# Kernel tuning notes

Hardware: AMD Instinct MI355X
Metric: run time of the kernel (lower is better)

The kernel has to match this reference:

```python
import jax, jax.numpy as jnp
import numpy as np

B, T, D, H = 4, 2048, 1024, 16
HD = D // H  # 64


def setup_inputs() -> dict:
    key = jax.random.key(0)
    k1, k2, k3 = jax.random.split(key, 3)
    x = jax.random.normal(k1, (B, T, D), dtype=jnp.float32)
    # xavier-uniform-ish scaling for stability
    W_qkv = jax.random.normal(k2, (3 * D, D), dtype=jnp.float32) * (1.0 / np.sqrt(D))
    W_proj = jax.random.normal(k3, (D, D), dtype=jnp.float32) * (1.0 / np.sqrt(D))
    b_proj = jnp.zeros((D,), dtype=jnp.float32)
    return {"x": x, "W_qkv": W_qkv, "W_proj": W_proj, "b_proj": b_proj}


def reference(x, W_qkv, W_proj, b_proj):
    Bx, Tx, C = x.shape
    qkv = x @ W_qkv.T                      # [B,T,3C]
    q, k, v = jnp.split(qkv, 3, axis=-1)
    # [B,T,C] -> [B,H,T,hd]
    def heads(t):
        return t.reshape(Bx, Tx, H, HD).transpose(0, 2, 1, 3)
    q, k, v = heads(q), heads(k), heads(v)
    scale = 1.0 / np.sqrt(HD)
    scores = jnp.einsum('bhqd,bhkd->bhqk', q, k) * scale  # [B,H,T,T]
    causal = jnp.tril(jnp.ones((Tx, Tx), dtype=bool))
    scores = jnp.where(causal, scores, jnp.finfo(scores.dtype).min)
    attn = jax.nn.softmax(scores, axis=-1)
    out = jnp.einsum('bhqk,bhkd->bhqd', attn, v)          # [B,H,T,hd]
    out = out.transpose(0, 2, 1, 3).reshape(Bx, Tx, C)    # [B,T,C]
    return out @ W_proj.T + b_proj
```

## Files before the change

kernel.cpp:

```cpp
#include <hip/hip_runtime.h>
#include <hip/hip_bf16.h>

#define B_  4
#define T_  2048
#define D_  1024
#define H_  16
#define HD_ 64
#define THREE_D (3 * D_)
#define TWO_D   (2 * D_)

typedef short s16x8 __attribute__((ext_vector_type(8)));
typedef float f32x4 __attribute__((ext_vector_type(4)));
typedef unsigned short u16;
typedef unsigned short u16x4 __attribute__((ext_vector_type(4)));

static __device__ __forceinline__ s16x8 load8(const u16* p) {
    return *reinterpret_cast<const s16x8*>(p);
}
static __device__ __forceinline__ u16 f2bf(float f) {
    __hip_bfloat16 h = __float2bfloat16(f);
    return *reinterpret_cast<u16*>(&h);
}
static __device__ __forceinline__ u16 bftrunc(float f) {
    unsigned u; __builtin_memcpy(&u, &f, 4); return (u16)(u >> 16);
}

static __device__ __forceinline__ void gload_lds16(const u16* g, u16* l) {
#if __has_builtin(__builtin_amdgcn_global_load_lds)
    __builtin_amdgcn_global_load_lds(
        (__attribute__((address_space(1))) void*)g,
        (__attribute__((address_space(3))) void*)l, 16, 0, 0);
#else
    *reinterpret_cast<s16x8*>(l) = load8(g);
#endif
}

__global__ __launch_bounds__(256) void cvt3_f32_bf16(
    const float* __restrict__ a, u16* __restrict__ oa, int na,
    const float* __restrict__ bsrc, u16* __restrict__ ob, int nb,
    const float* __restrict__ c, u16* __restrict__ oc, int nc)
{
    int i = (blockIdx.x * 256 + threadIdx.x) * 4;
    const float* s; u16* d;
    if (i < na)                { s = a;    d = oa; }
    else if ((i -= na) < nb)   { s = bsrc; d = ob; }
    else if ((i -= nb) < nc)   { s = c;    d = oc; }
    else return;
    const float4 f = *reinterpret_cast<const float4*>(s + i);
    u16x4 r;
    r.x = f2bf(f.x); r.y = f2bf(f.y); r.z = f2bf(f.z); r.w = f2bf(f.w);
    *reinterpret_cast<u16x4*>(d + i) = r;
}

template<int MODE>
__global__ __launch_bounds__(256) void gemm_bt128(
    const u16* __restrict__ A,
    const u16* __restrict__ Bm,
    void* __restrict__ Cv,
    const float* __restrict__ bias,
    int M, int N, int K, int lda, int ldb, int ldc,
    float qsc, u16* __restrict__ vt)
{
    const int ntiles = N >> 7;
    const int mt = blockIdx.x / ntiles;
    const int nt = blockIdx.x % ntiles;
    const int m0 = mt * 128, n0 = nt * 128;
    const int tid  = threadIdx.x;
    const int lane = tid & 63;
    const int l15  = lane & 15;
    const int quad = lane >> 4;
    const int wave = tid >> 6;
    const int wm = (wave >> 1) * 64;
    const int wn = (wave & 1) * 64;

    __shared__ u16 A_sh[2][128 * 32];
    __shared__ u16 B_sh[2][128 * 32];

    f32x4 acc[4][4] = {};

    const int c0 = tid, c1 = tid + 256;
    const int ar0 = c0 >> 2, as0 = (c0 & 3) * 8;
    const int ar1 = c1 >> 2, as1 = (c1 & 3) * 8;
    const u16* Ag0 = A  + (size_t)(m0 + ar0) * lda + as0;
    const u16* Ag1 = A  + (size_t)(m0 + ar1) * lda + as1;
    const u16* Bg0 = Bm + (size_t)(n0 + ar0) * ldb + as0;
    const u16* Bg1 = Bm + (size_t)(n0 + ar1) * ldb + as1;

    for (int k0 = 0; k0 < K; k0 += 64) {
        __syncthreads();
        #pragma unroll
        for (int p = 0; p < 2; ++p) {
            gload_lds16(Ag0 + k0 + p * 32, &A_sh[p][c0 * 8]);
            gload_lds16(Ag1 + k0 + p * 32, &A_sh[p][c1 * 8]);
            gload_lds16(Bg0 + k0 + p * 32, &B_sh[p][c0 * 8]);
            gload_lds16(Bg1 + k0 + p * 32, &B_sh[p][c1 * 8]);
        }
        __syncthreads();

        #pragma unroll
        for (int p = 0; p < 2; ++p) {
            s16x8 a[4], b[4];
            #pragma unroll
            for (int i = 0; i < 4; ++i) {
                a[i] = *reinterpret_cast<const s16x8*>(&A_sh[p][(wm + i * 16 + l15) * 32 + quad * 8]);
                b[i] = *reinterpret_cast<const s16x8*>(&B_sh[p][(wn + i * 16 + l15) * 32 + quad * 8]);
            }
            #pragma unroll
            for (int mi = 0; mi < 4; ++mi)
                #pragma unroll
                for (int ni = 0; ni < 4; ++ni)
                    acc[mi][ni] = __builtin_amdgcn_mfma_f32_16x16x32_bf16(
                        a[mi], b[ni], acc[mi][ni], 0, 0, 0);
        }
    }

    #pragma unroll
    for (int ni = 0; ni < 4; ++ni) {
        const int col = n0 + wn + ni * 16 + l15;
        if (MODE == 0) {
            const float bv = bias ? bias[col] : 0.0f;
            #pragma unroll
            for (int mi = 0; mi < 4; ++mi) {
                const int row = m0 + wm + mi * 16 + quad * 4;
                #pragma unroll
                for (int r = 0; r < 4; ++r)
                    ((float*)Cv)[(size_t)(row + r) * ldc + col] = acc[mi][ni][r] + bv;
            }
        } else {
            if (col < TWO_D) {
                const float sc = (col < D_) ? qsc : 1.0f;
                #pragma unroll
                for (int mi = 0; mi < 4; ++mi) {
                    const int row = m0 + wm + mi * 16 + quad * 4;
                    #pragma unroll
                    for (int r = 0; r < 4; ++r)
                        ((u16*)Cv)[(size_t)(row + r) * ldc + col] = f2bf(acc[mi][ni][r] * sc);
                }
            } else {
                const int vc = col - TWO_D;
                #pragma unroll
                for (int mi = 0; mi < 4; ++mi) {
                    const int row = m0 + wm + mi * 16 + quad * 4;
                    const int bb = row >> 11, t = row & (T_ - 1);
                    u16x4 pk;
                    #pragma unroll
                    for (int r = 0; r < 4; ++r) pk[r] = f2bf(acc[mi][ni][r]);
                    *reinterpret_cast<u16x4*>(
                        vt + ((size_t)(bb * H_ * HD_) + vc) * T_ + t) = pk;
                }
            }
        }
    }
}

__global__ __launch_bounds__(512) void flash_attn11(
    const u16* __restrict__ qk, const u16* __restrict__ vt,
    u16* __restrict__ out)
{
    const int cls = blockIdx.x >> 6;
    const int bh  = blockIdx.x & 63;
    const int qt  = 7 - cls;
    const int h = bh & 15, b = bh >> 4;
    const int q0 = qt * 256;

    __shared__ u16 K_lds[64 * 72];
    __shared__ u16 V_lds[64 * 72];
    __shared__ u16 P_lds[8 * 32 * 72];

    const int tid = threadIdx.x;
    const int wave = tid >> 6, lane = tid & 63;
    const int l15 = lane & 15, quad = lane >> 4;
    u16* Pw = P_lds + wave * (32 * 72);

    const int w0 = q0 + wave * 32;

    s16x8 qf[2][2];
    #pragma unroll
    for (int mi = 0; mi < 2; ++mi) {
        const size_t rowQ = (size_t)(b * T_ + w0 + mi * 16 + l15) * TWO_D + h * HD_;
        qf[mi][0] = load8(qk + rowQ + quad * 8);
        qf[mi][1] = load8(qk + rowQ + 32 + quad * 8);
    }

    f32x4 o[2][4] = {};
    f32x4 osum[2] = {};

    s16x8 ones;
    #pragma unroll
    for (int j = 0; j < 8; ++j) ones[j] = (short)0x3F80;

    const int rk = tid >> 3;
    const int s0 = (tid & 7) * 8;
    const u16* Kg = qk + (size_t)(b * T_ + rk) * TWO_D + D_ + h * HD_ + s0;
    const u16* Vg = vt + (size_t)(bh * HD_ + rk) * T_ + s0;

    s16x8 pk0 = load8(Kg);
    s16x8 pv0 = load8(Vg);

    const int nkt = 4 * qt + 4;
    for (int kt = 0; kt < nkt; ++kt) {
        const int kbase = kt * 64;
        __syncthreads();
        *reinterpret_cast<s16x8*>(&K_lds[rk * 72 + s0]) = pk0;
        *reinterpret_cast<s16x8*>(&V_lds[rk * 72 + s0]) = pv0;
        __syncthreads();

        if (kt + 1 < nkt) {
            const int nb = kbase + 64;
            pk0 = load8(Kg + (size_t)nb * TWO_D);
            pv0 = load8(Vg + nb);
        }

        if (kbase <= w0 + 31) {
            f32x4 st[2][4];
            #pragma unroll
            for (int n = 0; n < 4; ++n) {
                const s16x8 kf0 = *reinterpret_cast<const s16x8*>(
                    &K_lds[(n * 16 + l15) * 72 + quad * 8]);
                const s16x8 kf1 = *reinterpret_cast<const s16x8*>(
                    &K_lds[(n * 16 + l15) * 72 + 32 + quad * 8]);
                #pragma unroll
                for (int mi = 0; mi < 2; ++mi) {
                    f32x4 t = {};
                    t = __builtin_amdgcn_mfma_f32_16x16x32_bf16(kf0, qf[mi][0], t, 0, 0, 0);
                    t = __builtin_amdgcn_mfma_f32_16x16x32_bf16(kf1, qf[mi][1], t, 0, 0, 0);
                    st[mi][n] = t;
                }
            }

            const bool diag = (kbase + 63 > w0);
            #pragma unroll
            for (int mi = 0; mi < 2; ++mi) {
                const int qr = w0 + mi * 16 + l15;
                #pragma unroll
                for (int n = 0; n < 4; ++n) {
                    const int kb = kbase + n * 16 + quad * 4;
                    u16x4 pk;
                    #pragma unroll
                    for (int r = 0; r < 4; ++r)
                        pk[r] = bftrunc(exp2f(st[mi][n][r]));
                    if (diag) {
                        #pragma unroll
                        for (int r = 0; r < 4; ++r)
                            if (kb + r > qr) pk[r] = 0;
                    }
                    *reinterpret_cast<u16x4*>(
                        &Pw[(mi * 16 + l15) * 72 + n * 16 + quad * 4]) = pk;
                }
            }

            #pragma unroll
            for (int ks = 0; ks < 2; ++ks) {
                s16x8 pa[2];
                #pragma unroll
                for (int mi = 0; mi < 2; ++mi) {
                    pa[mi] = *reinterpret_cast<const s16x8*>(
                        &Pw[(mi * 16 + l15) * 72 + ks * 32 + quad * 8]);
                    osum[mi] = __builtin_amdgcn_mfma_f32_16x16x32_bf16(
                        pa[mi], ones, osum[mi], 0, 0, 0);
                }
                #pragma unroll
                for (int n4 = 0; n4 < 4; ++n4) {
                    const s16x8 vb = *reinterpret_cast<const s16x8*>(
                        &V_lds[(n4 * 16 + l15) * 72 + ks * 32 + quad * 8]);
                    #pragma unroll
                    for (int mi = 0; mi < 2; ++mi)
                        o[mi][n4] = __builtin_amdgcn_mfma_f32_16x16x32_bf16(
                            pa[mi], vb, o[mi][n4], 0, 0, 0);
                }
            }
        }
    }

    #pragma unroll
    for (int mi = 0; mi < 2; ++mi)
        #pragma unroll
        for (int r = 0; r < 4; ++r) {
            const float inv = 1.0f / osum[mi][r];
            const size_t rowO = (size_t)(b * T_ + w0 + mi * 16 + quad * 4 + r) * D_ + h * HD_;
            #pragma unroll
            for (int n4 = 0; n4 < 4; ++n4)
                out[rowO + n4 * 16 + l15] = f2bf(o[mi][n4][r] * inv);
        }
}

extern "C" void kernel_launch(void* const* d_in, const int* in_sizes, int n_in,
                              void* d_out, int out_size, void* d_ws, size_t ws_size,
                              hipStream_t stream)
{
    const float* x     = (const float*)d_in[0];
    const float* Wqkv  = (const float*)d_in[1];
    const float* Wproj = (const float*)d_in[2];
    const float* bproj = (const float*)d_in[3];
    float* out = (float*)d_out;

    const int M = B_ * T_;
    const float cs = 0.18033688011f;

    u16* xb    = (u16*)d_ws;
    u16* wqkvb = xb    + (size_t)M * D_;
    u16* wprob = wqkvb + (size_t)THREE_D * D_;
    u16* qk    = wprob + (size_t)D_ * D_;
    u16* vtb   = qk    + (size_t)M * TWO_D;
    u16* attn  = vtb   + (size_t)B_ * H_ * HD_ * T_;

    {
        const int na = M * D_, nb = THREE_D * D_, nc = D_ * D_;
        const int total = na + nb + nc;
        cvt3_f32_bf16<<<dim3((total / 4 + 255) / 256), 256, 0, stream>>>(
            x, xb, na, Wqkv, wqkvb, nb, Wproj, wprob, nc);
    }

    gemm_bt128<1><<<dim3((M / 128) * (THREE_D / 128)), 256, 0, stream>>>(
        xb, wqkvb, qk, nullptr, M, THREE_D, D_, D_, D_, TWO_D, cs, vtb);

    flash_attn11<<<dim3(B_ * H_ * (T_ / 256)), 512, 0, stream>>>(qk, vtb, attn);

    gemm_bt128<0><<<dim3((M / 128) * (D_ / 128)), 256, 0, stream>>>(
        attn, wprob, out, bproj, M, D_, D_, D_, D_, D_, 1.0f, nullptr);
}
```

Baseline: 255.7 us.

## Shrink attention tiles, XOR-swizzle K/V LDS, and remap GEMM blocks per XCD

The flash attention kernel moves from 256-row query tiles with 8 waves to 128-row tiles with 4 waves, doubling the block count. A snake-order query-tile map balances the causal work across blocks. K/V LDS tiles drop the 72-element padding in favour of an XOR swizzle to avoid bank conflicts, and each thread now loads two rows. The GEMM remaps block indices so that consecutive M tiles sit on the same XCD for L2 reuse. The cost is more blocks, each reloading K/V, and index arithmetic that assumes the tile count divides evenly by 8.

```diff
diff --git a/kernel.cpp b/kernel.cpp
--- a/kernel.cpp
+++ b/kernel.cpp
@@ -62,8 +62,13 @@
     float qsc, u16* __restrict__ vt)
 {
     const int ntiles = N >> 7;
-    const int mt = blockIdx.x / ntiles;
-    const int nt = blockIdx.x % ntiles;
+    const int nwg  = (M >> 7) * ntiles;
+    const int cpx  = nwg >> 3;
+    const int mtpc = cpx / ntiles;
+    const int xcd  = (int)blockIdx.x & 7;
+    const int lc   = (int)blockIdx.x >> 3;
+    const int nt = lc / mtpc;
+    const int mt = xcd * mtpc + (lc % mtpc);
     const int m0 = mt * 128, n0 = nt * 128;
     const int tid  = threadIdx.x;
     const int lane = tid & 63;
@@ -153,19 +158,20 @@
     }
 }
 
-__global__ __launch_bounds__(512) void flash_attn11(
+__global__ __launch_bounds__(256) void flash_attn6s(
     const u16* __restrict__ qk, const u16* __restrict__ vt,
     u16* __restrict__ out)
 {
     const int cls = blockIdx.x >> 6;
     const int bh  = blockIdx.x & 63;
-    const int qt  = 7 - cls;
+    const int qmap[16] = {15,14,13,12, 8,9,10,11, 7,6,5,4, 0,1,2,3};
+    const int qt = qmap[cls];
     const int h = bh & 15, b = bh >> 4;
-    const int q0 = qt * 256;
-
-    __shared__ u16 K_lds[64 * 72];
-    __shared__ u16 V_lds[64 * 72];
-    __shared__ u16 P_lds[8 * 32 * 72];
+    const int q0 = qt * 128;
+
+    __shared__ u16 K_lds[64 * 64];
+    __shared__ u16 V_lds[64 * 64];
+    __shared__ u16 P_lds[4 * 32 * 72];
 
     const int tid = threadIdx.x;
     const int wave = tid >> 6, lane = tid & 63;
@@ -189,26 +195,37 @@
     #pragma unroll
     for (int j = 0; j < 8; ++j) ones[j] = (short)0x3F80;
 
-    const int rk = tid >> 3;
+    const int r0 = tid >> 3;
     const int s0 = (tid & 7) * 8;
-    const u16* Kg = qk + (size_t)(b * T_ + rk) * TWO_D + D_ + h * HD_ + s0;
-    const u16* Vg = vt + (size_t)(bh * HD_ + rk) * T_ + s0;
-
-    s16x8 pk0 = load8(Kg);
-    s16x8 pv0 = load8(Vg);
-
-    const int nkt = 4 * qt + 4;
+    const int wsw = (((tid & 7) ^ (r0 & 7)) * 8);
+    const u16* Kg0 = qk + (size_t)(b * T_ + r0)      * TWO_D + D_ + h * HD_ + s0;
+    const u16* Kg1 = qk + (size_t)(b * T_ + r0 + 32) * TWO_D + D_ + h * HD_ + s0;
+    const u16* Vg0 = vt + (size_t)(bh * HD_ + r0)      * T_ + s0;
+    const u16* Vg1 = vt + (size_t)(bh * HD_ + r0 + 32) * T_ + s0;
+
+    s16x8 pk0 = load8(Kg0);
+    s16x8 pk1 = load8(Kg1);
+    s16x8 pv0 = load8(Vg0);
+    s16x8 pv1 = load8(Vg1);
+
+    const int rsw = l15 & 7;
+
+    const int nkt = 2 * qt + 2;
     for (int kt = 0; kt < nkt; ++kt) {
         const int kbase = kt * 64;
         __syncthreads();
-        *reinterpret_cast<s16x8*>(&K_lds[rk * 72 + s0]) = pk0;
-        *reinterpret_cast<s16x8*>(&V_lds[rk * 72 + s0]) = pv0;
+        *reinterpret_cast<s16x8*>(&K_lds[r0 * 64 + wsw])        = pk0;
+        *reinterpret_cast<s16x8*>(&K_lds[(r0 + 32) * 64 + wsw]) = pk1;
+        *reinterpret_cast<s16x8*>(&V_lds[r0 * 64 + wsw])        = pv0;
+        *reinterpret_cast<s16x8*>(&V_lds[(r0 + 32) * 64 + wsw]) = pv1;
         __syncthreads();
 
         if (kt + 1 < nkt) {
             const int nb = kbase + 64;
-            pk0 = load8(Kg + (size_t)nb * TWO_D);
-            pv0 = load8(Vg + nb);
+            pk0 = load8(Kg0 + (size_t)nb * TWO_D);
+            pk1 = load8(Kg1 + (size_t)nb * TWO_D);
+            pv0 = load8(Vg0 + nb);
+            pv1 = load8(Vg1 + nb);
         }
 
         if (kbase <= w0 + 31) {
@@ -216,9 +233,9 @@
             #pragma unroll
             for (int n = 0; n < 4; ++n) {
                 const s16x8 kf0 = *reinterpret_cast<const s16x8*>(
-                    &K_lds[(n * 16 + l15) * 72 + quad * 8]);
+                    &K_lds[(n * 16 + l15) * 64 + ((quad ^ rsw) * 8)]);
                 const s16x8 kf1 = *reinterpret_cast<const s16x8*>(
-                    &K_lds[(n * 16 + l15) * 72 + 32 + quad * 8]);
+                    &K_lds[(n * 16 + l15) * 64 + (((quad ^ 4) ^ rsw) * 8)]);
                 #pragma unroll
                 for (int mi = 0; mi < 2; ++mi) {
                     f32x4 t = {};
@@ -262,7 +279,7 @@
                 #pragma unroll
                 for (int n4 = 0; n4 < 4; ++n4) {
                     const s16x8 vb = *reinterpret_cast<const s16x8*>(
-                        &V_lds[(n4 * 16 + l15) * 72 + ks * 32 + quad * 8]);
+                        &V_lds[(n4 * 16 + l15) * 64 + (((ks * 4 + quad) ^ rsw) * 8)]);
                     #pragma unroll
                     for (int mi = 0; mi < 2; ++mi)
                         o[mi][n4] = __builtin_amdgcn_mfma_f32_16x16x32_bf16(
@@ -314,7 +331,7 @@
     gemm_bt128<1><<<dim3((M / 128) * (THREE_D / 128)), 256, 0, stream>>>(
         xb, wqkvb, qk, nullptr, M, THREE_D, D_, D_, D_, TWO_D, cs, vtb);
 
-    flash_attn11<<<dim3(B_ * H_ * (T_ / 256)), 512, 0, stream>>>(qk, vtb, attn);
+    flash_attn6s<<<dim3(B_ * H_ * (T_ / 128)), 256, 0, stream>>>(qk, vtb, attn);
 
     gemm_bt128<0><<<dim3((M / 128) * (D_ / 128)), 256, 0, stream>>>(
         attn, wprob, out, bproj, M, D_, D_, D_, D_, D_, 1.0f, nullptr);
```

Measured after the change: 243.7 us. 4.7% less time.
